# Kernel optimization log

Hardware: AMD Instinct MI355X
Metric: run time of the kernel (lower is better)

## Reference

```python
import jax, jax.numpy as jnp
import numpy as np

D_IN = 1024
D_OUT = 1024

def setup_inputs() -> dict:
    key = jax.random.key(0)
    k1, k2, k3, k4 = jax.random.split(key, 4)
    x = jax.random.normal(k1, (4, 2048, D_IN), dtype=jnp.float32)
    s = 1.0 / np.sqrt(D_IN)
    Wk = jax.random.normal(k2, (D_OUT, D_IN), dtype=jnp.float32) * s
    Wq = jax.random.normal(k3, (D_OUT, D_IN), dtype=jnp.float32) * s
    Wv = jax.random.normal(k4, (D_OUT, D_IN), dtype=jnp.float32) * s
    return {"x": x, "Wk": Wk, "Wq": Wq, "Wv": Wv}

def reference(x, Wk, Wq, Wv):
    # Note: original code applies k_w to produce 'weighted_q' and q_w for
    # 'weighted_k' (swapped names); we reproduce the exact math.
    b, s, _ = x.shape
    q = jnp.einsum('bsd,ed->bse', x, Wk)  # [B,S,d_out]
    k = jnp.einsum('bsd,ed->bse', x, Wq)  # [B,S,d_out]
    v = jnp.einsum('bsd,ed->bse', x, Wv)  # [B,S,d_out]
    scores = jnp.einsum('bqe,bke->bqk', q, k)  # [B,S,S]
    causal = jnp.triu(jnp.ones((s, s), dtype=bool), k=1)  # True = masked (future)
    scores = jnp.where(causal[None], -jnp.inf, scores)
    inv_sqrt_d = jnp.float32(1.0 / np.sqrt(Wk.shape[0]))
    attn = jax.nn.softmax(scores * inv_sqrt_d, axis=-1)
    return jnp.einsum('bqk,bke->bqe', attn, v)
```

## Files before the change

kernel.cpp:

```cpp
#include <hip/hip_runtime.h>
#include <hip/hip_bf16.h>
#include <stdint.h>

#define BATCH 4
#define SEQ   2048
#define DIN   1024
#define DOUT  1024
#define MTOT  (BATCH*SEQ)

typedef __attribute__((ext_vector_type(8))) short bf16x8;
typedef __attribute__((ext_vector_type(4))) float f32x4;

__device__ inline unsigned short f2bf(float f) {
  union { float f; unsigned u; } a; a.f = f;
  unsigned r = a.u + 0x7fffu + ((a.u >> 16) & 1u);
  return (unsigned short)(r >> 16);
}

__device__ inline void gload_lds16(const void* g, void* l) {
  __builtin_amdgcn_global_load_lds(
      (__attribute__((address_space(1))) void*)(uintptr_t)(g),
      (__attribute__((address_space(3))) void*)(uintptr_t)(l),
      16, 0, 0);
}

__global__ __launch_bounds__(256)
void convert_kernel(const float* __restrict__ x, const float* __restrict__ wk,
                    const float* __restrict__ wq, const float* __restrict__ wv,
                    unsigned short* __restrict__ xb, unsigned short* __restrict__ wkqb,
                    unsigned short* __restrict__ wvb) {
  const long NX = (long)MTOT * DIN;
  const long NW = (long)DOUT * DIN;
  long t = (long)blockIdx.x * blockDim.x + threadIdx.x;
  long off = t * 4;
  if (off >= NX + 3 * NW) return;
  const float* src; unsigned short* dst; long o;
  if (off < NX)            { src = x;  dst = xb;        o = off; }
  else if (off < NX + NW)  { src = wk; dst = wkqb;      o = off - NX; }
  else if (off < NX + 2*NW){ src = wq; dst = wkqb + NW; o = off - NX - NW; }
  else                     { src = wv; dst = wvb;       o = off - NX - 2*NW; }
  f32x4 v = *(const f32x4*)(src + o);
  unsigned p0 = (unsigned)f2bf(v[0]) | ((unsigned)f2bf(v[1]) << 16);
  unsigned p1 = (unsigned)f2bf(v[2]) | ((unsigned)f2bf(v[3]) << 16);
  uint2* d = (uint2*)(dst + o);
  *d = make_uint2(p0, p1);
}

#define BM 128
#define BN 128
#define BK 64

__global__ __launch_bounds__(256, 2)
void gemm_kernel(const unsigned short* __restrict__ A,
                 const unsigned short* __restrict__ Bw,
                 void* __restrict__ Cout,
                 int lda, int ldb, int ldc, int K,
                 long aBatch, long bBatch, long cBatch,
                 float scale, int outBf16, int tri, int klimit) {
  int bj = blockIdx.x, bi = blockIdx.y, b = blockIdx.z;
  if (tri && bj > bi) return;
  int Keff = K;
  if (klimit) { int km = (bi + 1) * BM; Keff = km < K ? km : K; }

  const unsigned short* Ab = A  + (long)b * aBatch + (long)bi * BM * lda;
  const unsigned short* Bb = Bw + (long)b * bBatch + (long)bj * BN * ldb;

  __shared__ unsigned short at[BM * BK];
  __shared__ unsigned short bt[BN * BK];

  const int tid  = threadIdx.x;
  const int lane = tid & 63;
  const int w    = tid >> 6;
  const int wm   = w >> 1;
  const int wn   = w & 1;

  f32x4 acc[4][4];
#pragma unroll
  for (int i = 0; i < 4; i++)
#pragma unroll
    for (int j = 0; j < 4; j++) acc[i][j] = (f32x4){0.f, 0.f, 0.f, 0.f};

  const int srow = lane >> 3;
  const int scol = (lane & 7) * 8;

  const int ntiles = Keff / BK;
  for (int kt = 0; kt < ntiles; ++kt) {
    const int k0 = kt * BK;
    if (kt) __syncthreads();
#pragma unroll
    for (int t = 0; t < 4; t++) {
      const int r = w * 32 + t * 8 + srow;
      gload_lds16(Ab + (long)r * lda + k0 + scol, &at[(w * 32 + t * 8) * BK + lane * 8]);
      gload_lds16(Bb + (long)r * ldb + k0 + scol, &bt[(w * 32 + t * 8) * BK + lane * 8]);
    }
    asm volatile("s_waitcnt vmcnt(0)" ::: "memory");
    __syncthreads();
#pragma unroll
    for (int kk = 0; kk < 2; ++kk) {
      bf16x8 af[4], bfr[4];
#pragma unroll
      for (int i = 0; i < 4; i++)
        af[i] = *(const bf16x8*)&at[(wm * 64 + i * 16 + (lane & 15)) * BK + kk * 32 + (lane >> 4) * 8];
#pragma unroll
      for (int j = 0; j < 4; j++)
        bfr[j] = *(const bf16x8*)&bt[(wn * 64 + j * 16 + (lane & 15)) * BK + kk * 32 + (lane >> 4) * 8];
#pragma unroll
      for (int i = 0; i < 4; i++)
#pragma unroll
        for (int j = 0; j < 4; j++)
          acc[i][j] = __builtin_amdgcn_mfma_f32_16x16x32_bf16(af[i], bfr[j], acc[i][j], 0, 0, 0);
    }
  }

  const long crow0 = (long)bi * BM + wm * 64;
  const long ccol0 = (long)bj * BN + wn * 64;
  if (outBf16) {
    unsigned short* C = (unsigned short*)Cout + (long)b * cBatch;
#pragma unroll
    for (int i = 0; i < 4; i++) {
      const long row0 = crow0 + i * 16 + ((lane >> 4) << 2);
#pragma unroll
      for (int j = 0; j < 4; j++) {
        const long col = ccol0 + j * 16 + (lane & 15);
#pragma unroll
        for (int r2 = 0; r2 < 4; r2++)
          C[(row0 + r2) * ldc + col] = f2bf(acc[i][j][r2] * scale);
      }
    }
  } else {
    float* C = (float*)Cout + (long)b * cBatch;
#pragma unroll
    for (int i = 0; i < 4; i++) {
      const long row0 = crow0 + i * 16 + ((lane >> 4) << 2);
#pragma unroll
      for (int j = 0; j < 4; j++) {
        const long col = ccol0 + j * 16 + (lane & 15);
#pragma unroll
        for (int r2 = 0; r2 < 4; r2++)
          C[(row0 + r2) * ldc + col] = acc[i][j][r2] * scale;
      }
    }
  }
}

__global__ __launch_bounds__(256)
void softmax_kernel(const float* __restrict__ scores, unsigned short* __restrict__ P) {
  __shared__ float rowbuf[SEQ];
  __shared__ float red[8];
  const int r = blockIdx.x;
  const int i = r & (SEQ - 1);
  const int n = i + 1;
  const int kend = ((i >> 7) + 1) << 7;
  const float* src = scores + (long)r * SEQ;
  unsigned short* dst = P + (long)r * SEQ;
  const int tid = threadIdx.x;

  float m = -1e30f;
  for (int j = tid; j < n; j += 256) { float v = src[j]; rowbuf[j] = v; m = fmaxf(m, v); }
#pragma unroll
  for (int o = 32; o; o >>= 1) m = fmaxf(m, __shfl_down(m, o, 64));
  if ((tid & 63) == 0) red[tid >> 6] = m;
  __syncthreads();
  m = fmaxf(fmaxf(red[0], red[1]), fmaxf(red[2], red[3]));

  float s = 0.f;
  for (int j = tid; j < n; j += 256) { float e = __expf(rowbuf[j] - m); rowbuf[j] = e; s += e; }
#pragma unroll
  for (int o = 32; o; o >>= 1) s += __shfl_down(s, o, 64);
  if ((tid & 63) == 0) red[4 + (tid >> 6)] = s;
  __syncthreads();
  s = red[4] + red[5] + red[6] + red[7];
  const float inv = 1.0f / s;

  for (int j = tid; j < n; j += 256) dst[j] = f2bf(rowbuf[j] * inv);
  for (int j = n + tid; j < kend; j += 256) dst[j] = 0;
}

extern "C" void kernel_launch(void* const* d_in, const int* in_sizes, int n_in,
                              void* d_out, int out_size, void* d_ws, size_t ws_size,
                              hipStream_t stream) {
  const float* x  = (const float*)d_in[0];
  const float* Wk = (const float*)d_in[1];
  const float* Wq = (const float*)d_in[2];
  const float* Wv = (const float*)d_in[3];

  char* ws = (char*)d_ws;
  unsigned short* xb   = (unsigned short*)(ws);
  unsigned short* qk   = (unsigned short*)(ws + 16777216);
  unsigned short* vtb  = (unsigned short*)(ws + 50331648);
  unsigned short* wkqb = (unsigned short*)(ws + 67108864);
  unsigned short* wvb  = (unsigned short*)(ws + 71303168);
  float*          scores = (float*)(ws + 73400320);
  unsigned short* P    = (unsigned short*)(ws + 140509184);
  float* out = (float*)d_out;

  {
    long total4 = ((long)MTOT * DIN + 3L * DOUT * DIN) / 4;
    int blocks = (int)((total4 + 255) / 256);
    convert_kernel<<<dim3(blocks), dim3(256), 0, stream>>>(x, Wk, Wq, Wv, xb, wkqb, wvb);
  }
  gemm_kernel<<<dim3(2048 / BN, 8192 / BM, 1), dim3(256), 0, stream>>>(
      xb, wkqb, qk, 1024, 1024, 2048, 1024, 0L, 0L, 0L, 1.0f, 1, 0, 0);
  gemm_kernel<<<dim3(8192 / BN, 1024 / BM, 1), dim3(256), 0, stream>>>(
      wvb, xb, vtb, 1024, 1024, 8192, 1024, 0L, 0L, 0L, 1.0f, 1, 0, 0);
  gemm_kernel<<<dim3(16, 16, BATCH), dim3(256), 0, stream>>>(
      qk, qk + 1024, scores, 2048, 2048, 2048, 1024,
      (long)SEQ * 2048, (long)SEQ * 2048, (long)SEQ * SEQ, 0.03125f, 0, 1, 0);
  softmax_kernel<<<dim3(BATCH * SEQ), dim3(256), 0, stream>>>(scores, P);
  gemm_kernel<<<dim3(1024 / BN, 2048 / BM, BATCH), dim3(256), 0, stream>>>(
      P, vtb, out, 2048, 8192, 1024, 2048,
      (long)SEQ * SEQ, 2048L, (long)SEQ * DOUT, 1.0f, 0, 0, 1);
}
```

Measured before the change: 287.8 us.

## Fuse QKV projection, pipeline GEMM, pack causal tiles, bf16 scores and warp softmax

Replaces the separate QK and V projection GEMMs with one fused QKV GEMM. That GEMM uses a 256x128 tile, triple-buffered LDS with an XOR swizzle, and setprio around the MFMAs, and is followed by a separate transpose of V. The scores GEMM launches only the lower-triangular tiles through a packed index and stores scores in bf16 instead of fp32, which halves score traffic. Softmax becomes one wavefront per row working in registers, with vectorized loads and stores. The PV GEMM remaps row blocks to balance the causal work. The trade-offs are an extra transpose pass and bf16 rounding of the scores before softmax.

```diff
diff --git a/kernel.cpp b/kernel.cpp
--- a/kernel.cpp
+++ b/kernel.cpp
@@ -10,11 +10,15 @@
 
 typedef __attribute__((ext_vector_type(8))) short bf16x8;
 typedef __attribute__((ext_vector_type(4))) float f32x4;
+typedef unsigned short ushort_t;
 
 __device__ inline unsigned short f2bf(float f) {
   union { float f; unsigned u; } a; a.f = f;
   unsigned r = a.u + 0x7fffu + ((a.u >> 16) & 1u);
   return (unsigned short)(r >> 16);
+}
+__device__ inline float bf2f(unsigned short b) {
+  union { unsigned u; float f; } a; a.u = ((unsigned)b) << 16; return a.f;
 }
 
 __device__ inline void gload_lds16(const void* g, void* l) {
@@ -46,6 +50,114 @@
   *d = make_uint2(p0, p1);
 }
 
+#define GBM 256
+#define GBN 128
+#define GBK 64
+
+__device__ inline void stage3(const unsigned short* __restrict__ Ab,
+                              const unsigned short* __restrict__ Bb,
+                              int lda, int ldb, int k0,
+                              unsigned short* at, unsigned short* bt, int tid) {
+#pragma unroll
+  for (int i = 0; i < 4; i++) {
+    int idx = i * 512 + tid;
+    int row = idx >> 3;
+    int cb  = (idx & 7) << 4;
+    int cbs = cb ^ ((row & 7) << 4);
+    gload_lds16((const char*)Ab + (long)row * (lda * 2) + k0 * 2 + cbs,
+                (char*)at + idx * 16);
+  }
+#pragma unroll
+  for (int i = 0; i < 2; i++) {
+    int idx = i * 512 + tid;
+    int row = idx >> 3;
+    int cb  = (idx & 7) << 4;
+    int cbs = cb ^ ((row & 7) << 4);
+    gload_lds16((const char*)Bb + (long)row * (ldb * 2) + k0 * 2 + cbs,
+                (char*)bt + idx * 16);
+  }
+}
+
+__device__ inline void compute3(const unsigned short* at, const unsigned short* bt,
+                                int lane, int wm, int wn, f32x4 acc[4][4]) {
+#pragma unroll
+  for (int kk = 0; kk < 2; kk++) {
+    bf16x8 af[4], bfr[4];
+#pragma unroll
+    for (int ii = 0; ii < 4; ii++) {
+      int row = wm * 64 + ii * 16 + (lane & 15);
+      int cb  = (kk * 64 + ((lane >> 4) << 4)) ^ ((row & 7) << 4);
+      af[ii] = *(const bf16x8*)((const char*)at + row * 128 + cb);
+    }
+#pragma unroll
+    for (int j = 0; j < 4; j++) {
+      int row = wn * 64 + j * 16 + (lane & 15);
+      int cb  = (kk * 64 + ((lane >> 4) << 4)) ^ ((row & 7) << 4);
+      bfr[j] = *(const bf16x8*)((const char*)bt + row * 128 + cb);
+    }
+    __builtin_amdgcn_s_setprio(1);
+#pragma unroll
+    for (int ii = 0; ii < 4; ii++)
+#pragma unroll
+      for (int j = 0; j < 4; j++)
+        acc[ii][j] = __builtin_amdgcn_mfma_f32_16x16x32_bf16(af[ii], bfr[j], acc[ii][j], 0, 0, 0);
+    __builtin_amdgcn_s_setprio(0);
+  }
+}
+
+__global__ __launch_bounds__(512, 2)
+void gemm3_kernel(const unsigned short* __restrict__ A,
+                  const unsigned short* __restrict__ Bw,
+                  unsigned short* __restrict__ C,
+                  int lda, int ldb, int ldc, int K) {
+  __shared__ unsigned short at[3][GBM * GBK];
+  __shared__ unsigned short bt[3][GBN * GBK];
+  const int bj = blockIdx.x, bi = blockIdx.y;
+  const unsigned short* Ab = A + (long)bi * GBM * lda;
+  const unsigned short* Bb = Bw + (long)bj * GBN * ldb;
+  const int tid = threadIdx.x, lane = tid & 63, w = tid >> 6;
+  const int wm = w >> 1, wn = w & 1;
+
+  f32x4 acc[4][4];
+#pragma unroll
+  for (int i = 0; i < 4; i++)
+#pragma unroll
+    for (int j = 0; j < 4; j++) acc[i][j] = (f32x4){0.f, 0.f, 0.f, 0.f};
+
+  const int nt = K / GBK;
+  unsigned short *a0 = at[0], *a1 = at[1], *a2 = at[2];
+  unsigned short *b0 = bt[0], *b1 = bt[1], *b2 = bt[2];
+
+  stage3(Ab, Bb, lda, ldb, 0,      a0, b0, tid);
+  stage3(Ab, Bb, lda, ldb, GBK,    a1, b1, tid);
+
+  for (int t = 0; t < nt; t++) {
+    if (t + 2 < nt) stage3(Ab, Bb, lda, ldb, (t + 2) * GBK, a2, b2, tid);
+    asm volatile("s_waitcnt vmcnt(12)" ::: "memory");
+    __builtin_amdgcn_s_barrier();
+    asm volatile("" ::: "memory");
+    compute3(a0, b0, lane, wm, wn, acc);
+    asm volatile("" ::: "memory");
+    __builtin_amdgcn_s_barrier();
+    unsigned short* ta = a0; a0 = a1; a1 = a2; a2 = ta;
+    unsigned short* tb = b0; b0 = b1; b1 = b2; b2 = tb;
+  }
+
+  const long crow0 = (long)bi * GBM + wm * 64;
+  const long ccol0 = (long)bj * GBN + wn * 64;
+#pragma unroll
+  for (int i = 0; i < 4; i++) {
+    const long row0 = crow0 + i * 16 + ((lane >> 4) << 2);
+#pragma unroll
+    for (int j = 0; j < 4; j++) {
+      const long col = ccol0 + j * 16 + (lane & 15);
+#pragma unroll
+      for (int r2 = 0; r2 < 4; r2++)
+        C[(row0 + r2) * ldc + col] = f2bf(acc[i][j][r2]);
+    }
+  }
+}
+
 #define BM 128
 #define BN 128
 #define BK 64
@@ -56,9 +168,21 @@
                  void* __restrict__ Cout,
                  int lda, int ldb, int ldc, int K,
                  long aBatch, long bBatch, long cBatch,
-                 float scale, int outBf16, int tri, int klimit) {
+                 float scale, int outBf16, int triPack, int klimit, int balance) {
   int bj = blockIdx.x, bi = blockIdx.y, b = blockIdx.z;
-  if (tri && bj > bi) return;
+  if (triPack) {
+    int idx = blockIdx.x;
+    int t = (int)((sqrtf(8.f * idx + 1.f) - 1.f) * 0.5f);
+    while ((t + 1) * (t + 2) / 2 <= idx) t++;
+    while (t * (t + 1) / 2 > idx) t--;
+    bi = t; bj = idx - t * (t + 1) / 2;
+  }
+  if (balance) {
+    int y = bi, h = y >> 1;
+    y = (y & 1) ? 15 - h : h;
+    if (b >= 2) y = 15 - y;
+    bi = y;
+  }
   int Keff = K;
   if (klimit) { int km = (bi + 1) * BM; Keff = km < K ? km : K; }
 
@@ -144,36 +268,83 @@
 }
 
 __global__ __launch_bounds__(256)
-void softmax_kernel(const float* __restrict__ scores, unsigned short* __restrict__ P) {
-  __shared__ float rowbuf[SEQ];
-  __shared__ float red[8];
-  const int r = blockIdx.x;
+void transpose_kernel(const unsigned short* __restrict__ qkv, unsigned short* __restrict__ vtb) {
+  __shared__ unsigned short lds[64][65];
+  const int m0 = blockIdx.x * 64, e0 = blockIdx.y * 64;
+  const int t = threadIdx.x;
+  const int r = t >> 3, c = (t & 7) * 8;
+#pragma unroll
+  for (int h = 0; h < 2; h++) {
+    const int rr = r + h * 32;
+    uint4 raw = *(const uint4*)(qkv + (long)(m0 + rr) * 3072 + 2048 + e0 + c);
+    const unsigned short* u = (const unsigned short*)&raw;
+#pragma unroll
+    for (int k = 0; k < 8; k++) lds[rr][c + k] = u[k];
+  }
+  __syncthreads();
+#pragma unroll
+  for (int h = 0; h < 2; h++) {
+    const int er = r + h * 32;
+    unsigned short v[8];
+#pragma unroll
+    for (int k = 0; k < 8; k++) v[k] = lds[c + k][er];
+    *(uint4*)(vtb + (long)(e0 + er) * 8192 + m0 + c) = *(const uint4*)v;
+  }
+}
+
+__global__ __launch_bounds__(256)
+void softmax_kernel(const unsigned short* __restrict__ scores, unsigned short* __restrict__ P) {
+  const int w = threadIdx.x >> 6, lane = threadIdx.x & 63;
+  const int r = blockIdx.x * 4 + w;
   const int i = r & (SEQ - 1);
-  const int n = i + 1;
   const int kend = ((i >> 7) + 1) << 7;
-  const float* src = scores + (long)r * SEQ;
+  const unsigned short* src = scores + (long)r * SEQ;
   unsigned short* dst = P + (long)r * SEQ;
-  const int tid = threadIdx.x;
-
+
+  float e[4][8];
   float m = -1e30f;
-  for (int j = tid; j < n; j += 256) { float v = src[j]; rowbuf[j] = v; m = fmaxf(m, v); }
-#pragma unroll
-  for (int o = 32; o; o >>= 1) m = fmaxf(m, __shfl_down(m, o, 64));
-  if ((tid & 63) == 0) red[tid >> 6] = m;
-  __syncthreads();
-  m = fmaxf(fmaxf(red[0], red[1]), fmaxf(red[2], red[3]));
+#pragma unroll
+  for (int c = 0; c < 4; c++) {
+    const int j0 = c * 512 + lane * 8;
+    if (j0 < kend) {
+      uint4 raw = *(const uint4*)(src + j0);
+      const unsigned short* u = (const unsigned short*)&raw;
+#pragma unroll
+      for (int k = 0; k < 8; k++) {
+        float v = bf2f(u[k]);
+        e[c][k] = (j0 + k <= i) ? v : -1e30f;
+        m = fmaxf(m, e[c][k]);
+      }
+    } else {
+#pragma unroll
+      for (int k = 0; k < 8; k++) e[c][k] = -1e30f;
+    }
+  }
+#pragma unroll
+  for (int o = 32; o; o >>= 1) m = fmaxf(m, __shfl_xor(m, o, 64));
 
   float s = 0.f;
-  for (int j = tid; j < n; j += 256) { float e = __expf(rowbuf[j] - m); rowbuf[j] = e; s += e; }
-#pragma unroll
-  for (int o = 32; o; o >>= 1) s += __shfl_down(s, o, 64);
-  if ((tid & 63) == 0) red[4 + (tid >> 6)] = s;
-  __syncthreads();
-  s = red[4] + red[5] + red[6] + red[7];
+#pragma unroll
+  for (int c = 0; c < 4; c++)
+#pragma unroll
+    for (int k = 0; k < 8; k++) {
+      float x = (e[c][k] > -1e29f) ? __expf(e[c][k] - m) : 0.f;
+      e[c][k] = x; s += x;
+    }
+#pragma unroll
+  for (int o = 32; o; o >>= 1) s += __shfl_xor(s, o, 64);
   const float inv = 1.0f / s;
 
-  for (int j = tid; j < n; j += 256) dst[j] = f2bf(rowbuf[j] * inv);
-  for (int j = n + tid; j < kend; j += 256) dst[j] = 0;
+#pragma unroll
+  for (int c = 0; c < 4; c++) {
+    const int j0 = c * 512 + lane * 8;
+    if (j0 < kend) {
+      unsigned short v[8];
+#pragma unroll
+      for (int k = 0; k < 8; k++) v[k] = f2bf(e[c][k] * inv);
+      *(uint4*)(dst + j0) = *(const uint4*)v;
+    }
+  }
 }
 
 extern "C" void kernel_launch(void* const* d_in, const int* in_sizes, int n_in,
@@ -185,29 +356,27 @@
   const float* Wv = (const float*)d_in[3];
 
   char* ws = (char*)d_ws;
-  unsigned short* xb   = (unsigned short*)(ws);
-  unsigned short* qk   = (unsigned short*)(ws + 16777216);
-  unsigned short* vtb  = (unsigned short*)(ws + 50331648);
-  unsigned short* wkqb = (unsigned short*)(ws + 67108864);
-  unsigned short* wvb  = (unsigned short*)(ws + 71303168);
-  float*          scores = (float*)(ws + 73400320);
-  unsigned short* P    = (unsigned short*)(ws + 140509184);
+  unsigned short* xb      = (unsigned short*)(ws);
+  unsigned short* qkv     = (unsigned short*)(ws + 16777216);
+  unsigned short* vtb     = (unsigned short*)(ws + 67108864);
+  unsigned short* wb      = (unsigned short*)(ws + 83886080);
+  unsigned short* scoresb = (unsigned short*)(ws + 90177536);
+  unsigned short* P       = (unsigned short*)(ws + 123731968);
   float* out = (float*)d_out;
 
   {
     long total4 = ((long)MTOT * DIN + 3L * DOUT * DIN) / 4;
     int blocks = (int)((total4 + 255) / 256);
-    convert_kernel<<<dim3(blocks), dim3(256), 0, stream>>>(x, Wk, Wq, Wv, xb, wkqb, wvb);
-  }
-  gemm_kernel<<<dim3(2048 / BN, 8192 / BM, 1), dim3(256), 0, stream>>>(
-      xb, wkqb, qk, 1024, 1024, 2048, 1024, 0L, 0L, 0L, 1.0f, 1, 0, 0);
-  gemm_kernel<<<dim3(8192 / BN, 1024 / BM, 1), dim3(256), 0, stream>>>(
-      wvb, xb, vtb, 1024, 1024, 8192, 1024, 0L, 0L, 0L, 1.0f, 1, 0, 0);
-  gemm_kernel<<<dim3(16, 16, BATCH), dim3(256), 0, stream>>>(
-      qk, qk + 1024, scores, 2048, 2048, 2048, 1024,
-      (long)SEQ * 2048, (long)SEQ * 2048, (long)SEQ * SEQ, 0.03125f, 0, 1, 0);
-  softmax_kernel<<<dim3(BATCH * SEQ), dim3(256), 0, stream>>>(scores, P);
+    convert_kernel<<<dim3(blocks), dim3(256), 0, stream>>>(x, Wk, Wq, Wv, xb, wb, wb + 2 * 1048576);
+  }
+  gemm3_kernel<<<dim3(3072 / GBN, 8192 / GBM), dim3(512), 0, stream>>>(
+      xb, wb, qkv, 1024, 1024, 3072, 1024);
+  transpose_kernel<<<dim3(8192 / 64, 1024 / 64), dim3(256), 0, stream>>>(qkv, vtb);
+  gemm_kernel<<<dim3(136, 1, BATCH), dim3(256), 0, stream>>>(
+      qkv, qkv + 1024, scoresb, 3072, 3072, 2048, 1024,
+      (long)SEQ * 3072, (long)SEQ * 3072, (long)SEQ * SEQ, 0.03125f, 1, 1, 0, 0);
+  softmax_kernel<<<dim3(BATCH * SEQ / 4), dim3(256), 0, stream>>>(scoresb, P);
   gemm_kernel<<<dim3(1024 / BN, 2048 / BM, BATCH), dim3(256), 0, stream>>>(
       P, vtb, out, 2048, 8192, 1024, 2048,
-      (long)SEQ * SEQ, 2048L, (long)SEQ * DOUT, 1.0f, 0, 0, 1);
-}
+      (long)SEQ * SEQ, 2048L, (long)SEQ * DOUT, 1.0f, 0, 0, 1, 1);
+}
```

After: 255.9 us. 1.12x faster.
